# Performance work log

Hardware: AMD Instinct MI355X
Metric: run time of the kernel (lower is better)

## Reference

```python
import jax, jax.numpy as jnp
import numpy as np

N_NODES = 100000
N_EDGES = 800000
N_GRAPHS = 512
C_IN = 32
N_CLASSES = 10


def setup_inputs() -> dict:
    key = jax.random.key(0)
    ks = jax.random.split(key, 12)
    x = jax.random.normal(ks[0], (N_NODES, C_IN), dtype=jnp.float32)
    edge_index = jax.random.randint(ks[1], (2, N_EDGES), 0, N_NODES, dtype=jnp.int64)
    batch = jnp.sort(jax.random.randint(ks[2], (N_NODES,), 0, N_GRAPHS, dtype=jnp.int64))
    # GCNConv weights initialized ~ N(0, 1/sqrt(in_channels)) per the source
    W1 = jax.random.normal(ks[3], (C_IN, 64), dtype=jnp.float32) / np.sqrt(C_IN).astype(np.float32)
    bc1 = jnp.zeros((64,), jnp.float32)
    W2 = jax.random.normal(ks[4], (64, 128), dtype=jnp.float32) / np.sqrt(64).astype(np.float32)
    bc2 = jnp.zeros((128,), jnp.float32)
    W3 = jax.random.normal(ks[5], (128, 256), dtype=jnp.float32) / np.sqrt(128).astype(np.float32)
    bc3 = jnp.zeros((256,), jnp.float32)
    Wlin = jnp.full((256, N_CLASSES), 0.01, jnp.float32)  # lin.weight filled with 0.01
    blin = jnp.zeros((N_CLASSES,), jnp.float32)
    return dict(x=x, edge_index=edge_index, batch=batch,
                W1=W1, bc1=bc1, W2=W2, bc2=bc2, W3=W3, bc3=bc3,
                Wlin=Wlin, blin=blin)


def _gcn_conv(x, W, b, src, dst, n_nodes):
    """PyG GCNConv: symmetric-normalized aggregation with self-loops.
    out = D^{-1/2} (A + I) D^{-1/2} (x W) + b
    """
    h = x @ W  # [N, F_out]
    ones_e = jnp.ones(src.shape, h.dtype)
    deg = jax.ops.segment_sum(ones_e, dst, num_segments=n_nodes) + 1.0  # self-loop included
    dinv = jax.lax.rsqrt(deg)
    norm = dinv[src] * dinv[dst]  # [E]
    agg = jax.ops.segment_sum(h[src] * norm[:, None], dst, num_segments=n_nodes)
    # self-loop contribution: norm_ii = dinv_i^2
    return agg + h * (dinv * dinv)[:, None] + b


def reference(x, edge_index, batch, W1, bc1, W2, bc2, W3, bc3, Wlin, blin):
    src, dst = edge_index[0], edge_index[1]
    h = jax.nn.relu(_gcn_conv(x, W1, bc1, src, dst, N_NODES))
    h = jax.nn.relu(_gcn_conv(h, W2, bc2, src, dst, N_NODES))
    h = _gcn_conv(h, W3, bc3, src, dst, N_NODES)  # no relu before pooling (matches source)
    # global mean pool over graphs
    summed = jax.ops.segment_sum(h, batch, num_segments=N_GRAPHS)  # [G, 256]
    counts = jax.ops.segment_sum(jnp.ones((N_NODES, 1), h.dtype), batch, num_segments=N_GRAPHS)
    pooled = summed / jnp.clip(counts, 1.0)
    return pooled @ Wlin + blin  # [G, num_classes]
```

## Files before the change

kernel.cpp:

```cpp
#include <hip/hip_runtime.h>
#include <hip/hip_bf16.h>


#define NN 100000
#define NE 800000
#define NG 512
#define PARTS 8

typedef unsigned int u32;

__device__ __forceinline__ u32 pack_bf2(float lo, float hi) {
    u32 ul = __float_as_uint(lo);
    u32 uh = __float_as_uint(hi);
    ul = (ul + 0x7fffu + ((ul >> 16) & 1u)) >> 16;
    uh = (uh + 0x7fffu + ((uh >> 16) & 1u)) & 0xffff0000u;
    return uh | ul;
}

#define BF_FMA8(ACC, V, W_) do { \
    (ACC)[0] += __uint_as_float((V).x << 16) * (W_); \
    (ACC)[1] += __uint_as_float((V).x & 0xffff0000u) * (W_); \
    (ACC)[2] += __uint_as_float((V).y << 16) * (W_); \
    (ACC)[3] += __uint_as_float((V).y & 0xffff0000u) * (W_); \
    (ACC)[4] += __uint_as_float((V).z << 16) * (W_); \
    (ACC)[5] += __uint_as_float((V).z & 0xffff0000u) * (W_); \
    (ACC)[6] += __uint_as_float((V).w << 16) * (W_); \
    (ACC)[7] += __uint_as_float((V).w & 0xffff0000u) * (W_); \
} while (0)

#define BF_FMA4(ACC, V, W_) do { \
    (ACC)[0] += __uint_as_float((V).x << 16) * (W_); \
    (ACC)[1] += __uint_as_float((V).x & 0xffff0000u) * (W_); \
    (ACC)[2] += __uint_as_float((V).y << 16) * (W_); \
    (ACC)[3] += __uint_as_float((V).y & 0xffff0000u) * (W_); \
} while (0)

#define FMA4(A, H, W_) do { (A).x += (H).x * (W_); (A).y += (H).y * (W_); \
                            (A).z += (H).z * (W_); (A).w += (H).w * (W_); } while (0)

__global__ __launch_bounds__(256) void xcast(const float* __restrict__ x,
                                             u32* __restrict__ xb, int n4) {
    int i = blockIdx.x * 256 + threadIdx.x;
    if (i >= n4) return;
    const float4 v = *reinterpret_cast<const float4*>(&x[i * 4]);
    *reinterpret_cast<uint2*>(&xb[i * 2]) =
        make_uint2(pack_bf2(v.x, v.y), pack_bf2(v.z, v.w));
}

__global__ __launch_bounds__(256) void deg_count(const int* __restrict__ dst,
                                                 int* __restrict__ deg, int nE) {
    int e = blockIdx.x * 256 + threadIdx.x;
    if (e < nE) atomicAdd(&deg[dst[e]], 1);
}

__global__ __launch_bounds__(256) void scanA(const int* __restrict__ deg,
                                             int* __restrict__ ex,
                                             int* __restrict__ bsum, int n) {
    __shared__ int sdata[256];
    const int t = threadIdx.x;
    const int base = blockIdx.x * 1024;
    const int idx = base + t * 4;
    int v[4];
#pragma unroll
    for (int k = 0; k < 4; ++k) v[k] = (idx + k < n) ? deg[idx + k] : 0;
    int ts = v[0] + v[1] + v[2] + v[3];
    sdata[t] = ts;
    __syncthreads();
    for (int off = 1; off < 256; off <<= 1) {
        int val = (t >= off) ? sdata[t - off] : 0;
        __syncthreads();
        sdata[t] += val;
        __syncthreads();
    }
    int run = sdata[t] - ts;
    if (t == 255) bsum[blockIdx.x] = sdata[255];
#pragma unroll
    for (int k = 0; k < 4; ++k) {
        if (idx + k < n) ex[idx + k] = run;
        run += v[k];
    }
}

__global__ __launch_bounds__(128) void scanB(int* __restrict__ bsum, int nb) {
    __shared__ int s[128];
    const int t = threadIdx.x;
    int orig = (t < nb) ? bsum[t] : 0;
    s[t] = orig;
    __syncthreads();
    for (int off = 1; off < 128; off <<= 1) {
        int val = (t >= off) ? s[t - off] : 0;
        __syncthreads();
        s[t] += val;
        __syncthreads();
    }
    if (t < nb) bsum[t] = s[t] - orig;
}

__global__ __launch_bounds__(256) void scanC(int* __restrict__ rp,
                                             const int* __restrict__ bsum,
                                             int* __restrict__ cursor,
                                             const int* __restrict__ deg,
                                             float* __restrict__ dinv,
                                             int n, int total) {
    int i = blockIdx.x * 256 + threadIdx.x;
    if (i < n) {
        int v = rp[i] + bsum[i >> 10];
        rp[i] = v;
        cursor[i] = v;
        dinv[i] = rsqrtf((float)deg[i] + 1.0f);
    }
    if (i == n) rp[n] = total;
}

__global__ __launch_bounds__(256) void fill_csr(const int* __restrict__ ei,
                                                const float* __restrict__ dinv,
                                                int* __restrict__ cursor,
                                                int2* __restrict__ cw, int nE) {
    int e = blockIdx.x * 256 + threadIdx.x;
    if (e >= nE) return;
    const int s = ei[e];
    const int d = ei[nE + e];
    const int pos = atomicAdd(&cursor[d], 1);
    const float wv = dinv[s] * dinv[d];
    cw[pos] = make_int2(s, __float_as_int(wv));
}

__global__ __launch_bounds__(256) void gather_gemm_l1(const u32* __restrict__ X,
                                                      const int* __restrict__ rp,
                                                      const int2* __restrict__ cw,
                                                      const float* __restrict__ dinv,
                                                      const float* __restrict__ W,
                                                      const float* __restrict__ bias,
                                                      u32* __restrict__ out, int n) {
    constexpr int AS = 36;
    __shared__ float agg[32 * AS];
    __shared__ float Wl[32 * 64];
    float4 wr[2];
#pragma unroll
    for (int i = 0; i < 2; ++i)
        wr[i] = *reinterpret_cast<const float4*>(&W[(threadIdx.x + i * 256) * 4]);

    const int nl = threadIdx.x >> 3;
    const int j = threadIdx.x & 7;
    const int node = blockIdx.x * 32 + nl;
    float a0[4], a1[4], a2[4], a3[4];
#pragma unroll
    for (int q = 0; q < 4; ++q) { a0[q] = 0.f; a1[q] = 0.f; a2[q] = 0.f; a3[q] = 0.f; }
    if (node < n) {
        const float di = dinv[node];
        const float c = di * di;
        const uint2 sv = *reinterpret_cast<const uint2*>(&X[(long long)node * 16 + j * 2]);
        BF_FMA4(a0, sv, c);
        int e = rp[node];
        const int end = rp[node + 1];
        for (; e + 4 <= end; e += 4) {
            const int2 c0 = cw[e], c1 = cw[e + 1], c2 = cw[e + 2], c3 = cw[e + 3];
            const uint2 h0 = *reinterpret_cast<const uint2*>(&X[(long long)c0.x * 16 + j * 2]);
            const uint2 h1 = *reinterpret_cast<const uint2*>(&X[(long long)c1.x * 16 + j * 2]);
            const uint2 h2 = *reinterpret_cast<const uint2*>(&X[(long long)c2.x * 16 + j * 2]);
            const uint2 h3 = *reinterpret_cast<const uint2*>(&X[(long long)c3.x * 16 + j * 2]);
            BF_FMA4(a0, h0, __int_as_float(c0.y));
            BF_FMA4(a1, h1, __int_as_float(c1.y));
            BF_FMA4(a2, h2, __int_as_float(c2.y));
            BF_FMA4(a3, h3, __int_as_float(c3.y));
        }
        if (e + 2 <= end) {
            const int2 c0 = cw[e], c1 = cw[e + 1];
            const uint2 h0 = *reinterpret_cast<const uint2*>(&X[(long long)c0.x * 16 + j * 2]);
            const uint2 h1 = *reinterpret_cast<const uint2*>(&X[(long long)c1.x * 16 + j * 2]);
            BF_FMA4(a0, h0, __int_as_float(c0.y));
            BF_FMA4(a1, h1, __int_as_float(c1.y));
            e += 2;
        }
        if (e < end) {
            const int2 c0 = cw[e];
            const uint2 h0 = *reinterpret_cast<const uint2*>(&X[(long long)c0.x * 16 + j * 2]);
            BF_FMA4(a0, h0, __int_as_float(c0.y));
        }
#pragma unroll
        for (int q = 0; q < 4; ++q) a0[q] += a1[q] + a2[q] + a3[q];
    }
    *reinterpret_cast<float4*>(&agg[nl * AS + j * 4]) =
        make_float4(a0[0], a0[1], a0[2], a0[3]);
#pragma unroll
    for (int i = 0; i < 2; ++i)
        *reinterpret_cast<float4*>(&Wl[(threadIdx.x + i * 256) * 4]) = wr[i];
    __syncthreads();

    const int r0 = (threadIdx.x >> 4) * 2;
    const int cg = (threadIdx.x & 15) * 4;
    float4 o0 = make_float4(0.f, 0.f, 0.f, 0.f);
    float4 o1 = o0;
#pragma unroll 8
    for (int k = 0; k < 32; ++k) {
        const float4 wv = *reinterpret_cast<const float4*>(&Wl[k * 64 + cg]);
        const float x0 = agg[r0 * AS + k];
        const float x1 = agg[(r0 + 1) * AS + k];
        FMA4(o0, wv, x0);
        FMA4(o1, wv, x1);
    }
    const float4 bv = *reinterpret_cast<const float4*>(&bias[cg]);
    o0.x = fmaxf(o0.x + bv.x, 0.f); o0.y = fmaxf(o0.y + bv.y, 0.f);
    o0.z = fmaxf(o0.z + bv.z, 0.f); o0.w = fmaxf(o0.w + bv.w, 0.f);
    o1.x = fmaxf(o1.x + bv.x, 0.f); o1.y = fmaxf(o1.y + bv.y, 0.f);
    o1.z = fmaxf(o1.z + bv.z, 0.f); o1.w = fmaxf(o1.w + bv.w, 0.f);
    const int row0 = blockIdx.x * 32 + r0;
    if (row0 < n)
        *reinterpret_cast<uint2*>(&out[(long long)row0 * 32 + (cg >> 1)]) =
            make_uint2(pack_bf2(o0.x, o0.y), pack_bf2(o0.z, o0.w));
    if (row0 + 1 < n)
        *reinterpret_cast<uint2*>(&out[(long long)(row0 + 1) * 32 + (cg >> 1)]) =
            make_uint2(pack_bf2(o1.x, o1.y), pack_bf2(o1.z, o1.w));
}

__global__ __launch_bounds__(256) void gather_gemm_l2(const u32* __restrict__ X,
                                                      const int* __restrict__ rp,
                                                      const int2* __restrict__ cw,
                                                      const float* __restrict__ dinv,
                                                      const float* __restrict__ W,
                                                      const float* __restrict__ bias,
                                                      u32* __restrict__ out, int n) {
    constexpr int AS = 68;
    __shared__ float agg[32 * AS];
    __shared__ float Wl[64 * 128];
    float4 wr[8];
#pragma unroll
    for (int i = 0; i < 8; ++i)
        wr[i] = *reinterpret_cast<const float4*>(&W[(threadIdx.x + i * 256) * 4]);

    const int nl = threadIdx.x >> 3;
    const int j = threadIdx.x & 7;
    const int node = blockIdx.x * 32 + nl;
    float a0[8], a1[8], a2[8], a3[8];
#pragma unroll
    for (int q = 0; q < 8; ++q) { a0[q] = 0.f; a1[q] = 0.f; a2[q] = 0.f; a3[q] = 0.f; }
    if (node < n) {
        const float di = dinv[node];
        const float c = di * di;
        const uint4 sv = *reinterpret_cast<const uint4*>(&X[(long long)node * 32 + j * 4]);
        BF_FMA8(a0, sv, c);
        int e = rp[node];
        const int end = rp[node + 1];
        for (; e + 4 <= end; e += 4) {
            const int2 c0 = cw[e], c1 = cw[e + 1], c2 = cw[e + 2], c3 = cw[e + 3];
            const uint4 h0 = *reinterpret_cast<const uint4*>(&X[(long long)c0.x * 32 + j * 4]);
            const uint4 h1 = *reinterpret_cast<const uint4*>(&X[(long long)c1.x * 32 + j * 4]);
            const uint4 h2 = *reinterpret_cast<const uint4*>(&X[(long long)c2.x * 32 + j * 4]);
            const uint4 h3 = *reinterpret_cast<const uint4*>(&X[(long long)c3.x * 32 + j * 4]);
            BF_FMA8(a0, h0, __int_as_float(c0.y));
            BF_FMA8(a1, h1, __int_as_float(c1.y));
            BF_FMA8(a2, h2, __int_as_float(c2.y));
            BF_FMA8(a3, h3, __int_as_float(c3.y));
        }
        if (e + 2 <= end) {
            const int2 c0 = cw[e], c1 = cw[e + 1];
            const uint4 h0 = *reinterpret_cast<const uint4*>(&X[(long long)c0.x * 32 + j * 4]);
            const uint4 h1 = *reinterpret_cast<const uint4*>(&X[(long long)c1.x * 32 + j * 4]);
            BF_FMA8(a0, h0, __int_as_float(c0.y));
            BF_FMA8(a1, h1, __int_as_float(c1.y));
            e += 2;
        }
        if (e < end) {
            const int2 c0 = cw[e];
            const uint4 h0 = *reinterpret_cast<const uint4*>(&X[(long long)c0.x * 32 + j * 4]);
            BF_FMA8(a0, h0, __int_as_float(c0.y));
        }
#pragma unroll
        for (int q = 0; q < 8; ++q) a0[q] += a1[q] + a2[q] + a3[q];
    }
    *reinterpret_cast<float4*>(&agg[nl * AS + j * 8]) =
        make_float4(a0[0], a0[1], a0[2], a0[3]);
    *reinterpret_cast<float4*>(&agg[nl * AS + j * 8 + 4]) =
        make_float4(a0[4], a0[5], a0[6], a0[7]);
#pragma unroll
    for (int i = 0; i < 8; ++i)
        *reinterpret_cast<float4*>(&Wl[(threadIdx.x + i * 256) * 4]) = wr[i];
    __syncthreads();

    const int r0 = (threadIdx.x >> 5) * 4;
    const int cg = (threadIdx.x & 31) * 4;
    float4 o0 = make_float4(0.f, 0.f, 0.f, 0.f);
    float4 o1 = o0, o2 = o0, o3 = o0;
#pragma unroll 8
    for (int k = 0; k < 64; ++k) {
        const float4 wv = *reinterpret_cast<const float4*>(&Wl[k * 128 + cg]);
        const float x0 = agg[(r0 + 0) * AS + k];
        const float x1 = agg[(r0 + 1) * AS + k];
        const float x2 = agg[(r0 + 2) * AS + k];
        const float x3 = agg[(r0 + 3) * AS + k];
        FMA4(o0, wv, x0);
        FMA4(o1, wv, x1);
        FMA4(o2, wv, x2);
        FMA4(o3, wv, x3);
    }
    const float4 bv = *reinterpret_cast<const float4*>(&bias[cg]);
    const int row0 = blockIdx.x * 32 + r0;
    float4 oo[4] = {o0, o1, o2, o3};
#pragma unroll
    for (int r = 0; r < 4; ++r) {
        float4 o = oo[r];
        o.x = fmaxf(o.x + bv.x, 0.f); o.y = fmaxf(o.y + bv.y, 0.f);
        o.z = fmaxf(o.z + bv.z, 0.f); o.w = fmaxf(o.w + bv.w, 0.f);
        if (row0 + r < n)
            *reinterpret_cast<uint2*>(&out[(long long)(row0 + r) * 64 + (cg >> 1)]) =
                make_uint2(pack_bf2(o.x, o.y), pack_bf2(o.z, o.w));
    }
}

__device__ __forceinline__ int lower_bound_i(const int* __restrict__ a, int n, int key) {
    int lo = 0, hi = n;
    while (lo < hi) {
        int mid = (lo + hi) >> 1;
        if (a[mid] < key) lo = mid + 1; else hi = mid;
    }
    return lo;
}

__global__ __launch_bounds__(256) void gather_pool(const u32* __restrict__ H,
                                                   const int* __restrict__ rp,
                                                   const int2* __restrict__ cw,
                                                   const float* __restrict__ dinv,
                                                   const int* __restrict__ batch,
                                                   float* __restrict__ Spart, int n) {
    __shared__ float red[16 * 128];
    const int g = blockIdx.x / PARTS;
    const int part = blockIdx.x % PARTS;
    const int slot = threadIdx.x >> 4;
    const int j = threadIdx.x & 15;
    const int start = lower_bound_i(batch, n, g);
    const int end = lower_bound_i(batch, n, g + 1);
    float a0[8], a1[8], a2[8], a3[8];
#pragma unroll
    for (int q = 0; q < 8; ++q) { a0[q] = 0.f; a1[q] = 0.f; a2[q] = 0.f; a3[q] = 0.f; }
    for (int node = start + part * 16 + slot; node < end; node += PARTS * 16) {
        const float di = dinv[node];
        const float c = di * di;
        const uint4 sv = *reinterpret_cast<const uint4*>(&H[(long long)node * 64 + j * 4]);
        BF_FMA8(a0, sv, c);
        int e = rp[node];
        const int eend = rp[node + 1];
        for (; e + 4 <= eend; e += 4) {
            const int2 c0 = cw[e], c1 = cw[e + 1], c2 = cw[e + 2], c3 = cw[e + 3];
            const uint4 h0 = *reinterpret_cast<const uint4*>(&H[(long long)c0.x * 64 + j * 4]);
            const uint4 h1 = *reinterpret_cast<const uint4*>(&H[(long long)c1.x * 64 + j * 4]);
            const uint4 h2 = *reinterpret_cast<const uint4*>(&H[(long long)c2.x * 64 + j * 4]);
            const uint4 h3 = *reinterpret_cast<const uint4*>(&H[(long long)c3.x * 64 + j * 4]);
            BF_FMA8(a0, h0, __int_as_float(c0.y));
            BF_FMA8(a1, h1, __int_as_float(c1.y));
            BF_FMA8(a2, h2, __int_as_float(c2.y));
            BF_FMA8(a3, h3, __int_as_float(c3.y));
        }
        if (e + 2 <= eend) {
            const int2 c0 = cw[e], c1 = cw[e + 1];
            const uint4 h0 = *reinterpret_cast<const uint4*>(&H[(long long)c0.x * 64 + j * 4]);
            const uint4 h1 = *reinterpret_cast<const uint4*>(&H[(long long)c1.x * 64 + j * 4]);
            BF_FMA8(a0, h0, __int_as_float(c0.y));
            BF_FMA8(a1, h1, __int_as_float(c1.y));
            e += 2;
        }
        if (e < eend) {
            const int2 c0 = cw[e];
            const uint4 h0 = *reinterpret_cast<const uint4*>(&H[(long long)c0.x * 64 + j * 4]);
            BF_FMA8(a0, h0, __int_as_float(c0.y));
        }
    }
#pragma unroll
    for (int q = 0; q < 8; ++q) a0[q] += a1[q] + a2[q] + a3[q];
    *reinterpret_cast<float4*>(&red[slot * 128 + j * 8]) =
        make_float4(a0[0], a0[1], a0[2], a0[3]);
    *reinterpret_cast<float4*>(&red[slot * 128 + j * 8 + 4]) =
        make_float4(a0[4], a0[5], a0[6], a0[7]);
    __syncthreads();
    const int t = threadIdx.x;
    if (t < 128) {
        float s = 0.f;
#pragma unroll
        for (int sl = 0; sl < 16; ++sl) s += red[sl * 128 + t];
        Spart[(long long)blockIdx.x * 128 + t] = s;
    }
}

__global__ __launch_bounds__(256) void final_k(const float* __restrict__ Spart,
                                               const int* __restrict__ batch,
                                               const float* __restrict__ W3,
                                               const float* __restrict__ b3,
                                               const float* __restrict__ Wlin,
                                               const float* __restrict__ blin,
                                               float* __restrict__ out, int n) {
    __shared__ float srow[128];
    __shared__ float prow[256];
    const int g = blockIdx.x;
    const int t = threadIdx.x;
    if (t < 128) {
        float s = 0.f;
#pragma unroll
        for (int p = 0; p < PARTS; ++p)
            s += Spart[(long long)(g * PARTS + p) * 128 + t];
        srow[t] = s;
    }
    __syncthreads();
    const int start = lower_bound_i(batch, n, g);
    const int end = lower_bound_i(batch, n, g + 1);
    const float cnt = (float)(end - start);
    const float inv = 1.0f / fmaxf(cnt, 1.0f);
    const float bscale = cnt * inv;
    float p = 0.f;
    for (int k = 0; k < 128; ++k) p += srow[k] * W3[k * 256 + t];
    prow[t] = p * inv + b3[t] * bscale;
    __syncthreads();
    if (t < 10) {
        float a = blin[t];
        for (int f = 0; f < 256; ++f) a += prow[f] * Wlin[f * 10 + t];
        out[g * 10 + t] = a;
    }
}

extern "C" void kernel_launch(void* const* d_in, const int* in_sizes, int n_in,
                              void* d_out, int out_size, void* d_ws, size_t ws_size,
                              hipStream_t stream) {
    const float* x     = (const float*)d_in[0];
    const int*   ei    = (const int*)d_in[1];
    const int*   batch = (const int*)d_in[2];
    const float* W1    = (const float*)d_in[3];
    const float* bc1   = (const float*)d_in[4];
    const float* W2    = (const float*)d_in[5];
    const float* bc2   = (const float*)d_in[6];
    const float* W3    = (const float*)d_in[7];
    const float* bc3   = (const float*)d_in[8];
    const float* Wlin  = (const float*)d_in[9];
    const float* blin  = (const float*)d_in[10];
    float* out = (float*)d_out;

    char* w = (char*)d_ws;
    int*   deg    = (int*)w;               w += 131072 * 4;
    int*   rp     = (int*)w;               w += 131072 * 4;
    int*   cursor = (int*)w;               w += 131072 * 4;
    int*   bsum   = (int*)w;               w += 256 * 4;
    float* dinv   = (float*)w;             w += 131072 * 4;
    int2*  cw     = (int2*)w;              w += (long long)NE * 8;
    u32*   xb     = (u32*)w;               w += (long long)NN * 16 * 4;
    u32*   Q      = (u32*)w;               w += (long long)NN * 32 * 4;
    u32*   P      = (u32*)w;               w += (long long)NN * 64 * 4;
    float* Spart  = (float*)w;             w += (long long)NG * PARTS * 128 * 4;

    const int nbScanA = (NN + 1023) / 1024;

    hipMemsetAsync(deg, 0, NN * sizeof(int), stream);
    xcast<<<(NN * 8 + 255) / 256, 256, 0, stream>>>(x, xb, NN * 8);
    deg_count<<<(NE + 255) / 256, 256, 0, stream>>>(ei + NE, deg, NE);
    scanA<<<nbScanA, 256, 0, stream>>>(deg, rp, bsum, NN);
    scanB<<<1, 128, 0, stream>>>(bsum, nbScanA);
    scanC<<<(NN + 256) / 256, 256, 0, stream>>>(rp, bsum, cursor, deg, dinv, NN, NE);
    fill_csr<<<(NE + 255) / 256, 256, 0, stream>>>(ei, dinv, cursor, cw, NE);

    gather_gemm_l1<<<(NN + 31) / 32, 256, 0, stream>>>(xb, rp, cw, dinv, W1, bc1, Q, NN);
    gather_gemm_l2<<<(NN + 31) / 32, 256, 0, stream>>>(Q, rp, cw, dinv, W2, bc2, P, NN);
    gather_pool<<<NG * PARTS, 256, 0, stream>>>(P, rp, cw, dinv, batch, Spart, NN);
    final_k<<<NG, 256, 0, stream>>>(Spart, batch, W3, bc3, Wlin, blin, out, NN);
}
```

Baseline: 238.9 us.

## Split pooling gather by feature slices instead of node partitions

```diff
diff --git a/kernel.cpp b/kernel.cpp
--- a/kernel.cpp
+++ b/kernel.cpp
@@ -5,7 +5,6 @@
 #define NN 100000
 #define NE 800000
 #define NG 512
-#define PARTS 8
 
 typedef unsigned int u32;
 
@@ -321,30 +320,31 @@
                                                    const int2* __restrict__ cw,
                                                    const float* __restrict__ dinv,
                                                    const int* __restrict__ batch,
-                                                   float* __restrict__ Spart, int n) {
-    __shared__ float red[16 * 128];
-    const int g = blockIdx.x / PARTS;
-    const int part = blockIdx.x % PARTS;
-    const int slot = threadIdx.x >> 4;
-    const int j = threadIdx.x & 15;
+                                                   float* __restrict__ S, int n) {
+    __shared__ float red[128 * 16 + 16 * 16];
+    const int s = blockIdx.x & 7;
+    const int g = blockIdx.x >> 3;
+    const int slot = threadIdx.x >> 1;
+    const int t2 = threadIdx.x & 1;
+    const int fo = s * 8 + t2 * 4;
     const int start = lower_bound_i(batch, n, g);
     const int end = lower_bound_i(batch, n, g + 1);
     float a0[8], a1[8], a2[8], a3[8];
 #pragma unroll
     for (int q = 0; q < 8; ++q) { a0[q] = 0.f; a1[q] = 0.f; a2[q] = 0.f; a3[q] = 0.f; }
-    for (int node = start + part * 16 + slot; node < end; node += PARTS * 16) {
+    for (int node = start + slot; node < end; node += 128) {
         const float di = dinv[node];
         const float c = di * di;
-        const uint4 sv = *reinterpret_cast<const uint4*>(&H[(long long)node * 64 + j * 4]);
+        const uint4 sv = *reinterpret_cast<const uint4*>(&H[(long long)node * 64 + fo]);
         BF_FMA8(a0, sv, c);
         int e = rp[node];
         const int eend = rp[node + 1];
         for (; e + 4 <= eend; e += 4) {
             const int2 c0 = cw[e], c1 = cw[e + 1], c2 = cw[e + 2], c3 = cw[e + 3];
-            const uint4 h0 = *reinterpret_cast<const uint4*>(&H[(long long)c0.x * 64 + j * 4]);
-            const uint4 h1 = *reinterpret_cast<const uint4*>(&H[(long long)c1.x * 64 + j * 4]);
-            const uint4 h2 = *reinterpret_cast<const uint4*>(&H[(long long)c2.x * 64 + j * 4]);
-            const uint4 h3 = *reinterpret_cast<const uint4*>(&H[(long long)c3.x * 64 + j * 4]);
+            const uint4 h0 = *reinterpret_cast<const uint4*>(&H[(long long)c0.x * 64 + fo]);
+            const uint4 h1 = *reinterpret_cast<const uint4*>(&H[(long long)c1.x * 64 + fo]);
+            const uint4 h2 = *reinterpret_cast<const uint4*>(&H[(long long)c2.x * 64 + fo]);
+            const uint4 h3 = *reinterpret_cast<const uint4*>(&H[(long long)c3.x * 64 + fo]);
             BF_FMA8(a0, h0, __int_as_float(c0.y));
             BF_FMA8(a1, h1, __int_as_float(c1.y));
             BF_FMA8(a2, h2, __int_as_float(c2.y));
@@ -352,35 +352,41 @@
         }
         if (e + 2 <= eend) {
             const int2 c0 = cw[e], c1 = cw[e + 1];
-            const uint4 h0 = *reinterpret_cast<const uint4*>(&H[(long long)c0.x * 64 + j * 4]);
-            const uint4 h1 = *reinterpret_cast<const uint4*>(&H[(long long)c1.x * 64 + j * 4]);
+            const uint4 h0 = *reinterpret_cast<const uint4*>(&H[(long long)c0.x * 64 + fo]);
+            const uint4 h1 = *reinterpret_cast<const uint4*>(&H[(long long)c1.x * 64 + fo]);
             BF_FMA8(a0, h0, __int_as_float(c0.y));
             BF_FMA8(a1, h1, __int_as_float(c1.y));
             e += 2;
         }
         if (e < eend) {
             const int2 c0 = cw[e];
-            const uint4 h0 = *reinterpret_cast<const uint4*>(&H[(long long)c0.x * 64 + j * 4]);
+            const uint4 h0 = *reinterpret_cast<const uint4*>(&H[(long long)c0.x * 64 + fo]);
             BF_FMA8(a0, h0, __int_as_float(c0.y));
         }
     }
 #pragma unroll
     for (int q = 0; q < 8; ++q) a0[q] += a1[q] + a2[q] + a3[q];
-    *reinterpret_cast<float4*>(&red[slot * 128 + j * 8]) =
+    *reinterpret_cast<float4*>(&red[slot * 16 + t2 * 8]) =
         make_float4(a0[0], a0[1], a0[2], a0[3]);
-    *reinterpret_cast<float4*>(&red[slot * 128 + j * 8 + 4]) =
+    *reinterpret_cast<float4*>(&red[slot * 16 + t2 * 8 + 4]) =
         make_float4(a0[4], a0[5], a0[6], a0[7]);
     __syncthreads();
-    const int t = threadIdx.x;
-    if (t < 128) {
-        float s = 0.f;
-#pragma unroll
-        for (int sl = 0; sl < 16; ++sl) s += red[sl * 128 + t];
-        Spart[(long long)blockIdx.x * 128 + t] = s;
-    }
-}
-
-__global__ __launch_bounds__(256) void final_k(const float* __restrict__ Spart,
+    const int grp = threadIdx.x >> 4;
+    const int ft = threadIdx.x & 15;
+    float s1 = 0.f;
+#pragma unroll
+    for (int k = 0; k < 8; ++k) s1 += red[(grp * 8 + k) * 16 + ft];
+    red[128 * 16 + grp * 16 + ft] = s1;
+    __syncthreads();
+    if (threadIdx.x < 16) {
+        float acc = 0.f;
+#pragma unroll
+        for (int k = 0; k < 16; ++k) acc += red[128 * 16 + k * 16 + threadIdx.x];
+        S[(long long)g * 128 + s * 16 + threadIdx.x] = acc;
+    }
+}
+
+__global__ __launch_bounds__(256) void final_k(const float* __restrict__ S,
                                                const int* __restrict__ batch,
                                                const float* __restrict__ W3,
                                                const float* __restrict__ b3,
@@ -391,13 +397,7 @@
     __shared__ float prow[256];
     const int g = blockIdx.x;
     const int t = threadIdx.x;
-    if (t < 128) {
-        float s = 0.f;
-#pragma unroll
-        for (int p = 0; p < PARTS; ++p)
-            s += Spart[(long long)(g * PARTS + p) * 128 + t];
-        srow[t] = s;
-    }
+    if (t < 128) srow[t] = S[(long long)g * 128 + t];
     __syncthreads();
     const int start = lower_bound_i(batch, n, g);
     const int end = lower_bound_i(batch, n, g + 1);
@@ -441,7 +441,7 @@
     u32*   xb     = (u32*)w;               w += (long long)NN * 16 * 4;
     u32*   Q      = (u32*)w;               w += (long long)NN * 32 * 4;
     u32*   P      = (u32*)w;               w += (long long)NN * 64 * 4;
-    float* Spart  = (float*)w;             w += (long long)NG * PARTS * 128 * 4;
+    float* S      = (float*)w;             w += (long long)NG * 128 * 4;
 
     const int nbScanA = (NN + 1023) / 1024;
 
@@ -455,6 +455,6 @@
 
     gather_gemm_l1<<<(NN + 31) / 32, 256, 0, stream>>>(xb, rp, cw, dinv, W1, bc1, Q, NN);
     gather_gemm_l2<<<(NN + 31) / 32, 256, 0, stream>>>(Q, rp, cw, dinv, W2, bc2, P, NN);
-    gather_pool<<<NG * PARTS, 256, 0, stream>>>(P, rp, cw, dinv, batch, Spart, NN);
-    final_k<<<NG, 256, 0, stream>>>(Spart, batch, W3, bc3, Wlin, blin, out, NN);
-}
+    gather_pool<<<NG * 8, 256, 0, stream>>>(P, rp, cw, dinv, batch, S, NN);
+    final_k<<<NG, 256, 0, stream>>>(S, batch, W3, bc3, Wlin, blin, out, NN);
+}
```

Result: slower. 304.6 us (+27.5%).

## Replace per-graph gather pooling with source-major scatter into shared graph accumulators

Applied to the files above, without the earlier changes.

```diff
diff --git a/kernel.cpp b/kernel.cpp
--- a/kernel.cpp
+++ b/kernel.cpp
@@ -5,9 +5,11 @@
 #define NN 100000
 #define NE 800000
 #define NG 512
-#define PARTS 8
+#define CCH 64
+#define CHSZ ((NN + CCH - 1) / CCH)
 
 typedef unsigned int u32;
+typedef unsigned long long u64;
 
 __device__ __forceinline__ u32 pack_bf2(float lo, float hi) {
     u32 ul = __float_as_uint(lo);
@@ -47,48 +49,56 @@
         make_uint2(pack_bf2(v.x, v.y), pack_bf2(v.z, v.w));
 }
 
-__global__ __launch_bounds__(256) void deg_count(const int* __restrict__ dst,
-                                                 int* __restrict__ deg, int nE) {
+__global__ __launch_bounds__(256) void deg_count2(const int* __restrict__ ei,
+                                                  int* __restrict__ deg_dst,
+                                                  int* __restrict__ deg_src, int nE) {
     int e = blockIdx.x * 256 + threadIdx.x;
-    if (e < nE) atomicAdd(&deg[dst[e]], 1);
-}
-
-__global__ __launch_bounds__(256) void scanA(const int* __restrict__ deg,
-                                             int* __restrict__ ex,
-                                             int* __restrict__ bsum, int n) {
-    __shared__ int sdata[256];
+    if (e >= nE) return;
+    atomicAdd(&deg_dst[ei[nE + e]], 1);
+    atomicAdd(&deg_src[ei[e]], 1);
+}
+
+__global__ __launch_bounds__(256) void scanA2(const int* __restrict__ dd,
+                                              const int* __restrict__ ds,
+                                              int* __restrict__ exd,
+                                              int* __restrict__ exs,
+                                              u64* __restrict__ bsum, int n) {
+    __shared__ u64 sdata[256];
     const int t = threadIdx.x;
-    const int base = blockIdx.x * 1024;
-    const int idx = base + t * 4;
-    int v[4];
-#pragma unroll
-    for (int k = 0; k < 4; ++k) v[k] = (idx + k < n) ? deg[idx + k] : 0;
-    int ts = v[0] + v[1] + v[2] + v[3];
+    const int idx = blockIdx.x * 1024 + t * 4;
+    u64 v[4];
+#pragma unroll
+    for (int k = 0; k < 4; ++k)
+        v[k] = (idx + k < n) ? ((u64)(u32)dd[idx + k] | ((u64)(u32)ds[idx + k] << 32)) : 0ull;
+    u64 ts = v[0] + v[1] + v[2] + v[3];
     sdata[t] = ts;
     __syncthreads();
     for (int off = 1; off < 256; off <<= 1) {
-        int val = (t >= off) ? sdata[t - off] : 0;
+        u64 val = (t >= off) ? sdata[t - off] : 0ull;
         __syncthreads();
         sdata[t] += val;
         __syncthreads();
     }
-    int run = sdata[t] - ts;
+    u64 run = sdata[t] - ts;
     if (t == 255) bsum[blockIdx.x] = sdata[255];
 #pragma unroll
     for (int k = 0; k < 4; ++k) {
-        if (idx + k < n) ex[idx + k] = run;
+        if (idx + k < n) {
+            exd[idx + k] = (int)(run & 0xffffffffull);
+            exs[idx + k] = (int)(run >> 32);
+        }
         run += v[k];
     }
 }
 
-__global__ __launch_bounds__(128) void scanB(int* __restrict__ bsum, int nb) {
-    __shared__ int s[128];
+__global__ __launch_bounds__(128) void scanB2(u64* __restrict__ bsum, int nb) {
+    __shared__ u64 s[128];
     const int t = threadIdx.x;
-    int orig = (t < nb) ? bsum[t] : 0;
+    u64 orig = (t < nb) ? bsum[t] : 0ull;
     s[t] = orig;
     __syncthreads();
     for (int off = 1; off < 128; off <<= 1) {
-        int val = (t >= off) ? s[t - off] : 0;
+        u64 val = (t >= off) ? s[t - off] : 0ull;
         __syncthreads();
         s[t] += val;
         __syncthreads();
@@ -96,33 +106,44 @@
     if (t < nb) bsum[t] = s[t] - orig;
 }
 
-__global__ __launch_bounds__(256) void scanC(int* __restrict__ rp,
-                                             const int* __restrict__ bsum,
-                                             int* __restrict__ cursor,
-                                             const int* __restrict__ deg,
-                                             float* __restrict__ dinv,
-                                             int n, int total) {
+__global__ __launch_bounds__(256) void scanC2(int* __restrict__ rpd,
+                                              int* __restrict__ rps,
+                                              const u64* __restrict__ bsum,
+                                              int* __restrict__ curd,
+                                              int* __restrict__ curs,
+                                              const int* __restrict__ degd,
+                                              float* __restrict__ dinv,
+                                              int n, int total) {
     int i = blockIdx.x * 256 + threadIdx.x;
     if (i < n) {
-        int v = rp[i] + bsum[i >> 10];
-        rp[i] = v;
-        cursor[i] = v;
-        dinv[i] = rsqrtf((float)deg[i] + 1.0f);
-    }
-    if (i == n) rp[n] = total;
-}
-
-__global__ __launch_bounds__(256) void fill_csr(const int* __restrict__ ei,
-                                                const float* __restrict__ dinv,
-                                                int* __restrict__ cursor,
-                                                int2* __restrict__ cw, int nE) {
+        const u64 b = bsum[i >> 10];
+        int vd = rpd[i] + (int)(b & 0xffffffffull);
+        int vs = rps[i] + (int)(b >> 32);
+        rpd[i] = vd; curd[i] = vd;
+        rps[i] = vs; curs[i] = vs;
+        dinv[i] = rsqrtf((float)degd[i] + 1.0f);
+    }
+    if (i == n) { rpd[n] = total; rps[n] = total; }
+}
+
+__global__ __launch_bounds__(256) void fill2(const int* __restrict__ ei,
+                                             const float* __restrict__ dinv,
+                                             const int* __restrict__ batch,
+                                             int* __restrict__ curd,
+                                             int* __restrict__ curs,
+                                             int2* __restrict__ cw,
+                                             u32* __restrict__ se, int nE) {
     int e = blockIdx.x * 256 + threadIdx.x;
     if (e >= nE) return;
     const int s = ei[e];
     const int d = ei[nE + e];
-    const int pos = atomicAdd(&cursor[d], 1);
     const float wv = dinv[s] * dinv[d];
-    cw[pos] = make_int2(s, __float_as_int(wv));
+    const int p1 = atomicAdd(&curd[d], 1);
+    cw[p1] = make_int2(s, __float_as_int(wv));
+    u32 uw = __float_as_uint(wv);
+    uw = (uw + 0x7fffu + ((uw >> 16) & 1u)) >> 16;
+    const int p2 = atomicAdd(&curs[s], 1);
+    se[p2] = ((u32)batch[d] << 16) | uw;
 }
 
 __global__ __launch_bounds__(256) void gather_gemm_l1(const u32* __restrict__ X,
@@ -295,6 +316,8 @@
     }
     const float4 bv = *reinterpret_cast<const float4*>(&bias[cg]);
     const int row0 = blockIdx.x * 32 + r0;
+    const int slice = cg >> 4;
+    const int within = (cg & 15) >> 1;
     float4 oo[4] = {o0, o1, o2, o3};
 #pragma unroll
     for (int r = 0; r < 4; ++r) {
@@ -302,9 +325,57 @@
         o.x = fmaxf(o.x + bv.x, 0.f); o.y = fmaxf(o.y + bv.y, 0.f);
         o.z = fmaxf(o.z + bv.z, 0.f); o.w = fmaxf(o.w + bv.w, 0.f);
         if (row0 + r < n)
-            *reinterpret_cast<uint2*>(&out[(long long)(row0 + r) * 64 + (cg >> 1)]) =
+            *reinterpret_cast<uint2*>(
+                &out[((long long)slice * n + (row0 + r)) * 8 + within]) =
                 make_uint2(pack_bf2(o.x, o.y), pack_bf2(o.z, o.w));
     }
+}
+
+__global__ __launch_bounds__(256) void pool_scatter(const u32* __restrict__ H,
+                                                    const int* __restrict__ rps,
+                                                    const u32* __restrict__ se,
+                                                    const float* __restrict__ dinv,
+                                                    const int* __restrict__ batch,
+                                                    float* __restrict__ Spart, int n) {
+    __shared__ float sp[512 * 17];
+    for (int i = threadIdx.x; i < 512 * 17; i += 256) sp[i] = 0.f;
+    __syncthreads();
+    const int slice = blockIdx.x & 7;
+    const int chunk = blockIdx.x >> 3;
+    const u32* Hs = H + (long long)slice * n * 8;
+    const int s0 = chunk * CHSZ;
+    const int s1 = (s0 + CHSZ < n) ? (s0 + CHSZ) : n;
+    for (int src = s0 + threadIdx.x; src < s1; src += 256) {
+        const uint4 r0 = *reinterpret_cast<const uint4*>(&Hs[(long long)src * 8]);
+        const uint4 r1 = *reinterpret_cast<const uint4*>(&Hs[(long long)src * 8 + 4]);
+        float h[16];
+        h[0] = __uint_as_float(r0.x << 16);  h[1] = __uint_as_float(r0.x & 0xffff0000u);
+        h[2] = __uint_as_float(r0.y << 16);  h[3] = __uint_as_float(r0.y & 0xffff0000u);
+        h[4] = __uint_as_float(r0.z << 16);  h[5] = __uint_as_float(r0.z & 0xffff0000u);
+        h[6] = __uint_as_float(r0.w << 16);  h[7] = __uint_as_float(r0.w & 0xffff0000u);
+        h[8] = __uint_as_float(r1.x << 16);  h[9] = __uint_as_float(r1.x & 0xffff0000u);
+        h[10] = __uint_as_float(r1.y << 16); h[11] = __uint_as_float(r1.y & 0xffff0000u);
+        h[12] = __uint_as_float(r1.z << 16); h[13] = __uint_as_float(r1.z & 0xffff0000u);
+        h[14] = __uint_as_float(r1.w << 16); h[15] = __uint_as_float(r1.w & 0xffff0000u);
+        const float di = dinv[src];
+        const float c = di * di;
+        const int gs = batch[src];
+#pragma unroll
+        for (int f = 0; f < 16; ++f) atomicAdd(&sp[gs * 17 + f], h[f] * c);
+        int e = rps[src];
+        const int ee = rps[src + 1];
+        for (; e < ee; ++e) {
+            const u32 m = se[e];
+            const int g = m >> 16;
+            const float wv = __uint_as_float(m << 16);
+#pragma unroll
+            for (int f = 0; f < 16; ++f) atomicAdd(&sp[g * 17 + f], h[f] * wv);
+        }
+    }
+    __syncthreads();
+    float* outp = &Spart[(long long)(slice * CCH + chunk) * (512 * 16)];
+    for (int i = threadIdx.x; i < 512 * 16; i += 256)
+        outp[i] = sp[(i >> 4) * 17 + (i & 15)];
 }
 
 __device__ __forceinline__ int lower_bound_i(const int* __restrict__ a, int n, int key) {
@@ -314,70 +385,6 @@
         if (a[mid] < key) lo = mid + 1; else hi = mid;
     }
     return lo;
-}
-
-__global__ __launch_bounds__(256) void gather_pool(const u32* __restrict__ H,
-                                                   const int* __restrict__ rp,
-                                                   const int2* __restrict__ cw,
-                                                   const float* __restrict__ dinv,
-                                                   const int* __restrict__ batch,
-                                                   float* __restrict__ Spart, int n) {
-    __shared__ float red[16 * 128];
-    const int g = blockIdx.x / PARTS;
-    const int part = blockIdx.x % PARTS;
-    const int slot = threadIdx.x >> 4;
-    const int j = threadIdx.x & 15;
-    const int start = lower_bound_i(batch, n, g);
-    const int end = lower_bound_i(batch, n, g + 1);
-    float a0[8], a1[8], a2[8], a3[8];
-#pragma unroll
-    for (int q = 0; q < 8; ++q) { a0[q] = 0.f; a1[q] = 0.f; a2[q] = 0.f; a3[q] = 0.f; }
-    for (int node = start + part * 16 + slot; node < end; node += PARTS * 16) {
-        const float di = dinv[node];
-        const float c = di * di;
-        const uint4 sv = *reinterpret_cast<const uint4*>(&H[(long long)node * 64 + j * 4]);
-        BF_FMA8(a0, sv, c);
-        int e = rp[node];
-        const int eend = rp[node + 1];
-        for (; e + 4 <= eend; e += 4) {
-            const int2 c0 = cw[e], c1 = cw[e + 1], c2 = cw[e + 2], c3 = cw[e + 3];
-            const uint4 h0 = *reinterpret_cast<const uint4*>(&H[(long long)c0.x * 64 + j * 4]);
-            const uint4 h1 = *reinterpret_cast<const uint4*>(&H[(long long)c1.x * 64 + j * 4]);
-            const uint4 h2 = *reinterpret_cast<const uint4*>(&H[(long long)c2.x * 64 + j * 4]);
-            const uint4 h3 = *reinterpret_cast<const uint4*>(&H[(long long)c3.x * 64 + j * 4]);
-            BF_FMA8(a0, h0, __int_as_float(c0.y));
-            BF_FMA8(a1, h1, __int_as_float(c1.y));
-            BF_FMA8(a2, h2, __int_as_float(c2.y));
-            BF_FMA8(a3, h3, __int_as_float(c3.y));
-        }
-        if (e + 2 <= eend) {
-            const int2 c0 = cw[e], c1 = cw[e + 1];
-            const uint4 h0 = *reinterpret_cast<const uint4*>(&H[(long long)c0.x * 64 + j * 4]);
-            const uint4 h1 = *reinterpret_cast<const uint4*>(&H[(long long)c1.x * 64 + j * 4]);
-            BF_FMA8(a0, h0, __int_as_float(c0.y));
-            BF_FMA8(a1, h1, __int_as_float(c1.y));
-            e += 2;
-        }
-        if (e < eend) {
-            const int2 c0 = cw[e];
-            const uint4 h0 = *reinterpret_cast<const uint4*>(&H[(long long)c0.x * 64 + j * 4]);
-            BF_FMA8(a0, h0, __int_as_float(c0.y));
-        }
-    }
-#pragma unroll
-    for (int q = 0; q < 8; ++q) a0[q] += a1[q] + a2[q] + a3[q];
-    *reinterpret_cast<float4*>(&red[slot * 128 + j * 8]) =
-        make_float4(a0[0], a0[1], a0[2], a0[3]);
-    *reinterpret_cast<float4*>(&red[slot * 128 + j * 8 + 4]) =
-        make_float4(a0[4], a0[5], a0[6], a0[7]);
-    __syncthreads();
-    const int t = threadIdx.x;
-    if (t < 128) {
-        float s = 0.f;
-#pragma unroll
-        for (int sl = 0; sl < 16; ++sl) s += red[sl * 128 + t];
-        Spart[(long long)blockIdx.x * 128 + t] = s;
-    }
 }
 
 __global__ __launch_bounds__(256) void final_k(const float* __restrict__ Spart,
@@ -392,10 +399,11 @@
     const int g = blockIdx.x;
     const int t = threadIdx.x;
     if (t < 128) {
+        const int slice = t >> 4;
+        const int within = t & 15;
         float s = 0.f;
-#pragma unroll
-        for (int p = 0; p < PARTS; ++p)
-            s += Spart[(long long)(g * PARTS + p) * 128 + t];
+        for (int c = 0; c < CCH; ++c)
+            s += Spart[(long long)(slice * CCH + c) * (512 * 16) + g * 16 + within];
         srow[t] = s;
     }
     __syncthreads();
@@ -432,29 +440,34 @@
     float* out = (float*)d_out;
 
     char* w = (char*)d_ws;
-    int*   deg    = (int*)w;               w += 131072 * 4;
-    int*   rp     = (int*)w;               w += 131072 * 4;
-    int*   cursor = (int*)w;               w += 131072 * 4;
-    int*   bsum   = (int*)w;               w += 256 * 4;
-    float* dinv   = (float*)w;             w += 131072 * 4;
-    int2*  cw     = (int2*)w;              w += (long long)NE * 8;
-    u32*   xb     = (u32*)w;               w += (long long)NN * 16 * 4;
-    u32*   Q      = (u32*)w;               w += (long long)NN * 32 * 4;
-    u32*   P      = (u32*)w;               w += (long long)NN * 64 * 4;
-    float* Spart  = (float*)w;             w += (long long)NG * PARTS * 128 * 4;
+    int*   deg_dst = (int*)w;              w += 131072 * 4;
+    int*   deg_src = (int*)w;              w += 131072 * 4;
+    int*   rpd     = (int*)w;              w += 131072 * 4;
+    int*   rps     = (int*)w;              w += 131072 * 4;
+    int*   curd    = (int*)w;              w += 131072 * 4;
+    int*   curs    = (int*)w;              w += 131072 * 4;
+    u64*   bsum    = (u64*)w;              w += 256 * 8;
+    float* dinv    = (float*)w;            w += 131072 * 4;
+    int2*  cw      = (int2*)w;             w += (long long)NE * 8;
+    u32*   se      = (u32*)w;              w += (long long)NE * 4;
+    u32*   xb      = (u32*)w;              w += (long long)NN * 16 * 4;
+    u32*   Q       = (u32*)w;              w += (long long)NN * 32 * 4;
+    u32*   P       = (u32*)w;              w += (long long)NN * 64 * 4;
+    float* Spart   = (float*)w;            w += (long long)8 * CCH * 512 * 16 * 4;
 
     const int nbScanA = (NN + 1023) / 1024;
 
-    hipMemsetAsync(deg, 0, NN * sizeof(int), stream);
+    hipMemsetAsync(deg_dst, 0, 2 * 131072 * sizeof(int), stream);
     xcast<<<(NN * 8 + 255) / 256, 256, 0, stream>>>(x, xb, NN * 8);
-    deg_count<<<(NE + 255) / 256, 256, 0, stream>>>(ei + NE, deg, NE);
-    scanA<<<nbScanA, 256, 0, stream>>>(deg, rp, bsum, NN);
-    scanB<<<1, 128, 0, stream>>>(bsum, nbScanA);
-    scanC<<<(NN + 256) / 256, 256, 0, stream>>>(rp, bsum, cursor, deg, dinv, NN, NE);
-    fill_csr<<<(NE + 255) / 256, 256, 0, stream>>>(ei, dinv, cursor, cw, NE);
-
-    gather_gemm_l1<<<(NN + 31) / 32, 256, 0, stream>>>(xb, rp, cw, dinv, W1, bc1, Q, NN);
-    gather_gemm_l2<<<(NN + 31) / 32, 256, 0, stream>>>(Q, rp, cw, dinv, W2, bc2, P, NN);
-    gather_pool<<<NG * PARTS, 256, 0, stream>>>(P, rp, cw, dinv, batch, Spart, NN);
+    deg_count2<<<(NE + 255) / 256, 256, 0, stream>>>(ei, deg_dst, deg_src, NE);
+    scanA2<<<nbScanA, 256, 0, stream>>>(deg_dst, deg_src, rpd, rps, bsum, NN);
+    scanB2<<<1, 128, 0, stream>>>(bsum, nbScanA);
+    scanC2<<<(NN + 256) / 256, 256, 0, stream>>>(rpd, rps, bsum, curd, curs,
+                                                 deg_dst, dinv, NN, NE);
+    fill2<<<(NE + 255) / 256, 256, 0, stream>>>(ei, dinv, batch, curd, curs, cw, se, NE);
+
+    gather_gemm_l1<<<(NN + 31) / 32, 256, 0, stream>>>(xb, rpd, cw, dinv, W1, bc1, Q, NN);
+    gather_gemm_l2<<<(NN + 31) / 32, 256, 0, stream>>>(Q, rpd, cw, dinv, W2, bc2, P, NN);
+    pool_scatter<<<CCH * 8, 256, 0, stream>>>(P, rps, se, dinv, batch, Spart, NN);
     final_k<<<NG, 256, 0, stream>>>(Spart, batch, W3, bc3, Wlin, blin, out, NN);
 }
```

Result: slower. 861.3 us (+260.6%).
